# Kernel optimization log

Hardware: AMD Instinct MI355X
Metric: run time of the kernel (lower is better)

Reference implementation:

```python
import jax, jax.numpy as jnp
import numpy as np


def setup_inputs() -> dict:
    key = jax.random.key(0)
    k1, k2 = jax.random.split(key)
    # [1, D, H, W, C] cubic feature volume
    image_features = jax.random.normal(k1, (1, 64, 64, 64, 64), dtype=jnp.float32)
    # [1, N, 3] vertex coords in the original 128^3 volume, in [0, 128)
    graph_features = jax.random.uniform(k2, (1, 200000, 3), dtype=jnp.float32) * 128.0
    return {"image_features": image_features, "graph_features": graph_features}


def reference(image_features, graph_features):
    img = image_features[0]                      # [D, H, W, C]
    H = img.shape[0]
    factor = jnp.float32(128.0 / H)
    x = graph_features[..., -3] / factor         # [B, N]
    y = graph_features[..., -2] / factor
    z = graph_features[..., -1] / factor
    hm1 = jnp.float32(H - 1)
    x1 = jnp.floor(x); x2 = jnp.minimum(jnp.ceil(x), hm1)
    y1 = jnp.floor(y); y2 = jnp.minimum(jnp.ceil(y), hm1)
    z1 = jnp.floor(z); z2 = jnp.minimum(jnp.ceil(z), hm1)

    def gather(ix, iy, iz):
        # [B, N] index arrays -> [B, N, C] gathered features
        return img[ix.astype(jnp.int32), iy.astype(jnp.int32), iz.astype(jnp.int32)]

    wx = (x - x1)[..., None]; wx2 = (x2 - x)[..., None]
    wy = (y - y1)[..., None]; wy2 = (y2 - y)[..., None]
    wz = (z - z1)[..., None]; wz2 = (z2 - z)[..., None]

    # z = z1 plane
    q11 = gather(x1, y1, z1); q21 = gather(x2, y1, z1)
    q12 = gather(x1, y2, z1); q22 = gather(x2, y2, z1)
    lerp_y1 = (q22 * wx + q12 * wx2) * wy + (q21 * wx + q11 * wx2) * wy2

    # z = z2 plane
    q11 = gather(x1, y1, z2); q21 = gather(x2, y1, z2)
    q12 = gather(x1, y2, z2); q22 = gather(x2, y2, z2)
    lerp_y2 = (q22 * wx + q12 * wx2) * wy + (q21 * wx + q11 * wx2) * wy2

    return lerp_y2 * wz + lerp_y1 * wz2          # [B, N, C]
```

## Files before the change

kernel.cpp:

```cpp
#include <hip/hip_runtime.h>


#define NBUCK   4096
#define CAP     128
#define OVCAP   8192
#define TILE_F4 2048

typedef float __attribute__((ext_vector_type(4))) fx4;

#define GLOBAL_AS __attribute__((address_space(1)))
#define LDS_AS    __attribute__((address_space(3)))

__device__ __forceinline__ void async_copy16(const float4* g, float4* l) {
    __builtin_amdgcn_global_load_lds(
        (const GLOBAL_AS unsigned int*)(const void*)g,
        (LDS_AS unsigned int*)(void*)l, 16, 0, 0);
}

__device__ __forceinline__ float4 f4mul(float4 a, float s) {
    return make_float4(a.x * s, a.y * s, a.z * s, a.w * s);
}
__device__ __forceinline__ float4 f4fma(float4 a, float s, float4 acc) {
    return make_float4(fmaf(a.x, s, acc.x), fmaf(a.y, s, acc.y),
                       fmaf(a.z, s, acc.z), fmaf(a.w, s, acc.w));
}

__global__ __launch_bounds__(256) void scatter_kernel(
    const float* __restrict__ coords, int* __restrict__ counts,
    float4* __restrict__ buckets, float4* __restrict__ overflow, int n)
{
    int p = blockIdx.x * 256 + threadIdx.x;
    if (p >= n) return;
    float xs = coords[3 * p + 0] * 0.5f;
    float ys = coords[3 * p + 1] * 0.5f;
    float zs = coords[3 * p + 2] * 0.5f;
    int vx = (int)floorf(xs), vy = (int)floorf(ys), vz = (int)floorf(zs);
    int bucket = ((vx >> 2) << 8) | ((vy >> 2) << 4) | (vz >> 2);
    int slot = atomicAdd(&counts[bucket], 1);
    float4 v = make_float4(xs, ys, zs, __int_as_float(p));
    if (slot < CAP) {
        buckets[bucket * CAP + slot] = v;
    } else {
        int o = atomicAdd(&counts[NBUCK], 1);
        if (o < OVCAP) overflow[o] = v;
    }
}

__global__ __launch_bounds__(256) void gather_kernel(
    const float* __restrict__ img, const int* __restrict__ counts,
    const float4* __restrict__ buckets, const float4* __restrict__ overflow,
    float* __restrict__ out)
{
    const float4* __restrict__ imgv = (const float4*)img;
    int cvec = threadIdx.x & 15;
    int grp  = threadIdx.x >> 4;

    if (blockIdx.x < NBUCK) {
        __shared__ float4 tile[TILE_F4];
        int bucket = (blockIdx.x & 7) * 512 + (blockIdx.x >> 3);
        int bx0 = (bucket >> 8) << 2;
        int by0 = ((bucket >> 4) & 15) << 2;
        int bz0 = (bucket & 15) << 2;

        {
            int wv   = threadIdx.x >> 6;
            int lane = threadIdx.x & 63;
            #pragma unroll
            for (int c = 0; c < 8; c++) {
                int f = ((wv << 3) + c) * 64 + lane;
                int tv = f >> 4;
                int ch = f & 15;
                tv = min(tv, 124);
                int lx = tv / 25;
                int rem = tv - lx * 25;
                int ly = rem / 5;
                int lz = rem - ly * 5;
                int gx = min(bx0 + lx, 63);
                int gy = min(by0 + ly, 63);
                int gz = min(bz0 + lz, 63);
                const float4* src = &imgv[(((((gx << 6) + gy) << 6) + gz) << 4) + ch];
                async_copy16(src, &tile[((wv << 3) + c) * 64]);
            }
        }
        int cnt = min(counts[bucket], CAP);
        __syncthreads();

        for (int i = grp; i < cnt; i += 16) {
            float4 cs = buckets[bucket * CAP + i];
            float x = cs.x, y = cs.y, z = cs.z;
            int p = __float_as_int(cs.w);

            float fx1 = floorf(x), fx2 = fminf(ceilf(x), 63.0f);
            float fy1 = floorf(y), fy2 = fminf(ceilf(y), 63.0f);
            float fz1 = floorf(z), fz2 = fminf(ceilf(z), 63.0f);

            int lx1 = (int)fx1 - bx0, lx2 = (int)fx2 - bx0;
            int ly1 = (int)fy1 - by0, ly2 = (int)fy2 - by0;
            int lz1 = (int)fz1 - bz0, lz2 = (int)fz2 - bz0;
            int ax1 = lx1 * 25, ax2 = lx2 * 25;
            int ay1 = ly1 * 5,  ay2 = ly2 * 5;

            float4 q111 = tile[((ax1 + ay1 + lz1) << 4) + cvec];
            float4 q211 = tile[((ax2 + ay1 + lz1) << 4) + cvec];
            float4 q121 = tile[((ax1 + ay2 + lz1) << 4) + cvec];
            float4 q221 = tile[((ax2 + ay2 + lz1) << 4) + cvec];
            float4 q112 = tile[((ax1 + ay1 + lz2) << 4) + cvec];
            float4 q212 = tile[((ax2 + ay1 + lz2) << 4) + cvec];
            float4 q122 = tile[((ax1 + ay2 + lz2) << 4) + cvec];
            float4 q222 = tile[((ax2 + ay2 + lz2) << 4) + cvec];

            float wx = x - fx1, wxc = fx2 - x;
            float wy = y - fy1, wyc = fy2 - y;
            float wz = z - fz1, wzc = fz2 - z;

            float4 ly1v = f4fma(f4fma(q221, wx, f4mul(q121, wxc)), wy,
                                f4mul(f4fma(q211, wx, f4mul(q111, wxc)), wyc));
            float4 ly2v = f4fma(f4fma(q222, wx, f4mul(q122, wxc)), wy,
                                f4mul(f4fma(q212, wx, f4mul(q112, wxc)), wyc));
            float4 res = f4fma(ly2v, wz, f4mul(ly1v, wzc));

            fx4 r; r.x = res.x; r.y = res.y; r.z = res.z; r.w = res.w;
            __builtin_nontemporal_store(r, (fx4*)out + (p << 4) + cvec);
        }
    } else {
        int ob = blockIdx.x - NBUCK;
        int cnt = min(counts[NBUCK], OVCAP);
        for (int i = (ob << 4) + grp; i < cnt; i += 32 * 16) {
            float4 cs = overflow[i];
            float x = cs.x, y = cs.y, z = cs.z;
            int p = __float_as_int(cs.w);

            float fx1 = floorf(x), fx2 = fminf(ceilf(x), 63.0f);
            float fy1 = floorf(y), fy2 = fminf(ceilf(y), 63.0f);
            float fz1 = floorf(z), fz2 = fminf(ceilf(z), 63.0f);

            int bx1 = ((int)fx1) << 12, bx2 = ((int)fx2) << 12;
            int by1 = ((int)fy1) << 6,  by2 = ((int)fy2) << 6;
            int iz1 = (int)fz1, iz2 = (int)fz2;

            float4 q111 = imgv[((bx1 + by1 + iz1) << 4) + cvec];
            float4 q211 = imgv[((bx2 + by1 + iz1) << 4) + cvec];
            float4 q121 = imgv[((bx1 + by2 + iz1) << 4) + cvec];
            float4 q221 = imgv[((bx2 + by2 + iz1) << 4) + cvec];
            float4 q112 = imgv[((bx1 + by1 + iz2) << 4) + cvec];
            float4 q212 = imgv[((bx2 + by1 + iz2) << 4) + cvec];
            float4 q122 = imgv[((bx1 + by2 + iz2) << 4) + cvec];
            float4 q222 = imgv[((bx2 + by2 + iz2) << 4) + cvec];

            float wx = x - fx1, wxc = fx2 - x;
            float wy = y - fy1, wyc = fy2 - y;
            float wz = z - fz1, wzc = fz2 - z;

            float4 ly1v = f4fma(f4fma(q221, wx, f4mul(q121, wxc)), wy,
                                f4mul(f4fma(q211, wx, f4mul(q111, wxc)), wyc));
            float4 ly2v = f4fma(f4fma(q222, wx, f4mul(q122, wxc)), wy,
                                f4mul(f4fma(q212, wx, f4mul(q112, wxc)), wyc));
            float4 res = f4fma(ly2v, wz, f4mul(ly1v, wzc));

            fx4 r; r.x = res.x; r.y = res.y; r.z = res.z; r.w = res.w;
            __builtin_nontemporal_store(r, (fx4*)out + (p << 4) + cvec);
        }
    }
}

__global__ __launch_bounds__(256) void trilerp_kernel(
    const float* __restrict__ img, const float* __restrict__ coords,
    float* __restrict__ out, int n_points)
{
    int tid = blockIdx.x * 256 + threadIdx.x;
    int p = tid >> 4;
    if (p >= n_points) return;
    int cvec = tid & 15;

    float x = coords[3 * p + 0] * 0.5f;
    float y = coords[3 * p + 1] * 0.5f;
    float z = coords[3 * p + 2] * 0.5f;

    float fx1 = floorf(x), fx2 = fminf(ceilf(x), 63.0f);
    float fy1 = floorf(y), fy2 = fminf(ceilf(y), 63.0f);
    float fz1 = floorf(z), fz2 = fminf(ceilf(z), 63.0f);

    float wx = x - fx1, wxc = fx2 - x;
    float wy = y - fy1, wyc = fy2 - y;
    float wz = z - fz1, wzc = fz2 - z;

    const float4* __restrict__ imgv = (const float4*)img;
    int bx1 = ((int)fx1) << 12, bx2 = ((int)fx2) << 12;
    int by1 = ((int)fy1) << 6,  by2 = ((int)fy2) << 6;
    int iz1 = (int)fz1, iz2 = (int)fz2;

    float4 q11 = imgv[((bx1 + by1 + iz1) << 4) + cvec];
    float4 q21 = imgv[((bx2 + by1 + iz1) << 4) + cvec];
    float4 q12 = imgv[((bx1 + by2 + iz1) << 4) + cvec];
    float4 q22 = imgv[((bx2 + by2 + iz1) << 4) + cvec];
    float4 ly1 = f4fma(f4fma(q22, wx, f4mul(q12, wxc)), wy,
                       f4mul(f4fma(q21, wx, f4mul(q11, wxc)), wyc));

    q11 = imgv[((bx1 + by1 + iz2) << 4) + cvec];
    q21 = imgv[((bx2 + by1 + iz2) << 4) + cvec];
    q12 = imgv[((bx1 + by2 + iz2) << 4) + cvec];
    q22 = imgv[((bx2 + by2 + iz2) << 4) + cvec];
    float4 ly2 = f4fma(f4fma(q22, wx, f4mul(q12, wxc)), wy,
                       f4mul(f4fma(q21, wx, f4mul(q11, wxc)), wyc));

    float4 res = f4fma(ly2, wz, f4mul(ly1, wzc));
    ((float4*)out)[(p << 4) + cvec] = res;
}

extern "C" void kernel_launch(void* const* d_in, const int* in_sizes, int n_in,
                              void* d_out, int out_size, void* d_ws, size_t ws_size,
                              hipStream_t stream) {
    const float* img    = (const float*)d_in[0];
    const float* coords = (const float*)d_in[1];
    float* out = (float*)d_out;
    int n = in_sizes[1] / 3;

    size_t counts_bytes = 32768;
    size_t buckets_off  = counts_bytes;
    size_t buckets_bytes = (size_t)NBUCK * CAP * sizeof(float4);
    size_t overflow_off = buckets_off + buckets_bytes;
    size_t need = overflow_off + (size_t)OVCAP * sizeof(float4);

    if (ws_size >= need) {
        int*    counts   = (int*)d_ws;
        float4* buckets  = (float4*)((char*)d_ws + buckets_off);
        float4* overflow = (float4*)((char*)d_ws + overflow_off);

        hipMemsetAsync(counts, 0, (NBUCK + 1) * sizeof(int), stream);
        int pgrid = (n + 255) / 256;
        scatter_kernel<<<pgrid, 256, 0, stream>>>(coords, counts, buckets, overflow, n);
        gather_kernel<<<NBUCK + 32, 256, 0, stream>>>(img, counts, buckets, overflow, out);
    } else {
        int threads = n * 16;
        int grid = (threads + 255) / 256;
        trilerp_kernel<<<grid, 256, 0, stream>>>(img, coords, out, n);
    }
}
```

Measured before the change: 142.0 us.

## Make gather blocks persistent over eight buckets with double-buffered async LDS staging

Each gather block now handles eight consecutive buckets with 512 threads, staging the next bucket's 5x5x5 voxel tile into a second LDS buffer while the current bucket is interpolated. Manual vmcnt waits and barriers replace the per-block __syncthreads. The aim is to hide the global-to-LDS load latency and cut per-block launch and setup overhead. In exchange the grid is much smaller (544 blocks instead of 4128), the LDS footprint doubles, and correctness relies on the hand-written waitcnt count. The trilinear code on the overflow and fallback paths is moved into a shared helper.

```diff
diff --git a/kernel.cpp b/kernel.cpp
--- a/kernel.cpp
+++ b/kernel.cpp
@@ -5,6 +5,8 @@
 #define CAP     128
 #define OVCAP   8192
 #define TILE_F4 2048
+#define NGB     512
+#define NB_PER  8
 
 typedef float __attribute__((ext_vector_type(4))) fx4;
 
@@ -46,7 +48,70 @@
     }
 }
 
-__global__ __launch_bounds__(256) void gather_kernel(
+__device__ __forceinline__ void stage_bucket(
+    const float4* __restrict__ imgv, int bucket, float4* dst,
+    int wv, int lane)
+{
+    int bx0 = (bucket >> 8) << 2;
+    int by0 = ((bucket >> 4) & 15) << 2;
+    int bz0 = (bucket & 15) << 2;
+    #pragma unroll
+    for (int c = 0; c < 4; c++) {
+        int chunk = (wv << 2) + c;
+        int f = chunk * 64 + lane;
+        int tv = min(f >> 4, 124);
+        int ch = f & 15;
+        int lx = tv / 25;
+        int rem = tv - lx * 25;
+        int ly = rem / 5;
+        int lz = rem - ly * 5;
+        int gx = min(bx0 + lx, 63);
+        int gy = min(by0 + ly, 63);
+        int gz = min(bz0 + lz, 63);
+        const float4* src = &imgv[(((((gx << 6) + gy) << 6) + gz) << 4) + ch];
+        async_copy16(src, dst + chunk * 64);
+    }
+}
+
+__device__ __forceinline__ void lerp_global_store(
+    const float4* __restrict__ imgv, float4 cs, int cvec,
+    float* __restrict__ out)
+{
+    float x = cs.x, y = cs.y, z = cs.z;
+    int p = __float_as_int(cs.w);
+
+    float fx1 = floorf(x), fx2 = fminf(ceilf(x), 63.0f);
+    float fy1 = floorf(y), fy2 = fminf(ceilf(y), 63.0f);
+    float fz1 = floorf(z), fz2 = fminf(ceilf(z), 63.0f);
+
+    int bx1 = ((int)fx1) << 12, bx2 = ((int)fx2) << 12;
+    int by1 = ((int)fy1) << 6,  by2 = ((int)fy2) << 6;
+    int iz1 = (int)fz1, iz2 = (int)fz2;
+
+    float4 q111 = imgv[((bx1 + by1 + iz1) << 4) + cvec];
+    float4 q211 = imgv[((bx2 + by1 + iz1) << 4) + cvec];
+    float4 q121 = imgv[((bx1 + by2 + iz1) << 4) + cvec];
+    float4 q221 = imgv[((bx2 + by2 + iz1) << 4) + cvec];
+    float4 q112 = imgv[((bx1 + by1 + iz2) << 4) + cvec];
+    float4 q212 = imgv[((bx2 + by1 + iz2) << 4) + cvec];
+    float4 q122 = imgv[((bx1 + by2 + iz2) << 4) + cvec];
+    float4 q222 = imgv[((bx2 + by2 + iz2) << 4) + cvec];
+
+    float wx = x - fx1, wxc = fx2 - x;
+    float wy = y - fy1, wyc = fy2 - y;
+    float wz = z - fz1, wzc = fz2 - z;
+
+    float4 ly1v = f4fma(f4fma(q221, wx, f4mul(q121, wxc)), wy,
+                        f4mul(f4fma(q211, wx, f4mul(q111, wxc)), wyc));
+    float4 ly2v = f4fma(f4fma(q222, wx, f4mul(q122, wxc)), wy,
+                        f4mul(f4fma(q212, wx, f4mul(q112, wxc)), wyc));
+    float4 res = f4fma(ly2v, wz, f4mul(ly1v, wzc));
+
+    fx4 r; r.x = res.x; r.y = res.y; r.z = res.z; r.w = res.w;
+    __builtin_nontemporal_store(r, (fx4*)out + (p << 4) + cvec);
+}
+
+__global__ __launch_bounds__(512) void gather_kernel(
     const float* __restrict__ img, const int* __restrict__ counts,
     const float4* __restrict__ buckets, const float4* __restrict__ overflow,
     float* __restrict__ out)
@@ -55,110 +120,77 @@
     int cvec = threadIdx.x & 15;
     int grp  = threadIdx.x >> 4;
 
-    if (blockIdx.x < NBUCK) {
-        __shared__ float4 tile[TILE_F4];
-        int bucket = (blockIdx.x & 7) * 512 + (blockIdx.x >> 3);
-        int bx0 = (bucket >> 8) << 2;
-        int by0 = ((bucket >> 4) & 15) << 2;
-        int bz0 = (bucket & 15) << 2;
-
-        {
-            int wv   = threadIdx.x >> 6;
-            int lane = threadIdx.x & 63;
-            #pragma unroll
-            for (int c = 0; c < 8; c++) {
-                int f = ((wv << 3) + c) * 64 + lane;
-                int tv = f >> 4;
-                int ch = f & 15;
-                tv = min(tv, 124);
-                int lx = tv / 25;
-                int rem = tv - lx * 25;
-                int ly = rem / 5;
-                int lz = rem - ly * 5;
-                int gx = min(bx0 + lx, 63);
-                int gy = min(by0 + ly, 63);
-                int gz = min(bz0 + lz, 63);
-                const float4* src = &imgv[(((((gx << 6) + gy) << 6) + gz) << 4) + ch];
-                async_copy16(src, &tile[((wv << 3) + c) * 64]);
+    if (blockIdx.x < NGB) {
+        __shared__ float4 tile[2][TILE_F4];
+        int wv   = threadIdx.x >> 6;
+        int lane = threadIdx.x & 63;
+        int bbase = (blockIdx.x & 7) * 512 + (blockIdx.x >> 3) * NB_PER;
+
+        stage_bucket(imgv, bbase, tile[0], wv, lane);
+
+        for (int i = 0; i < NB_PER; ++i) {
+            float4* cur = tile[i & 1];
+            if (i + 1 < NB_PER) {
+                stage_bucket(imgv, bbase + i + 1, tile[(i + 1) & 1], wv, lane);
+                asm volatile("s_waitcnt vmcnt(4)" ::: "memory");
+            } else {
+                asm volatile("s_waitcnt vmcnt(0)" ::: "memory");
             }
-        }
-        int cnt = min(counts[bucket], CAP);
-        __syncthreads();
-
-        for (int i = grp; i < cnt; i += 16) {
-            float4 cs = buckets[bucket * CAP + i];
-            float x = cs.x, y = cs.y, z = cs.z;
-            int p = __float_as_int(cs.w);
-
-            float fx1 = floorf(x), fx2 = fminf(ceilf(x), 63.0f);
-            float fy1 = floorf(y), fy2 = fminf(ceilf(y), 63.0f);
-            float fz1 = floorf(z), fz2 = fminf(ceilf(z), 63.0f);
-
-            int lx1 = (int)fx1 - bx0, lx2 = (int)fx2 - bx0;
-            int ly1 = (int)fy1 - by0, ly2 = (int)fy2 - by0;
-            int lz1 = (int)fz1 - bz0, lz2 = (int)fz2 - bz0;
-            int ax1 = lx1 * 25, ax2 = lx2 * 25;
-            int ay1 = ly1 * 5,  ay2 = ly2 * 5;
-
-            float4 q111 = tile[((ax1 + ay1 + lz1) << 4) + cvec];
-            float4 q211 = tile[((ax2 + ay1 + lz1) << 4) + cvec];
-            float4 q121 = tile[((ax1 + ay2 + lz1) << 4) + cvec];
-            float4 q221 = tile[((ax2 + ay2 + lz1) << 4) + cvec];
-            float4 q112 = tile[((ax1 + ay1 + lz2) << 4) + cvec];
-            float4 q212 = tile[((ax2 + ay1 + lz2) << 4) + cvec];
-            float4 q122 = tile[((ax1 + ay2 + lz2) << 4) + cvec];
-            float4 q222 = tile[((ax2 + ay2 + lz2) << 4) + cvec];
-
-            float wx = x - fx1, wxc = fx2 - x;
-            float wy = y - fy1, wyc = fy2 - y;
-            float wz = z - fz1, wzc = fz2 - z;
-
-            float4 ly1v = f4fma(f4fma(q221, wx, f4mul(q121, wxc)), wy,
-                                f4mul(f4fma(q211, wx, f4mul(q111, wxc)), wyc));
-            float4 ly2v = f4fma(f4fma(q222, wx, f4mul(q122, wxc)), wy,
-                                f4mul(f4fma(q212, wx, f4mul(q112, wxc)), wyc));
-            float4 res = f4fma(ly2v, wz, f4mul(ly1v, wzc));
-
-            fx4 r; r.x = res.x; r.y = res.y; r.z = res.z; r.w = res.w;
-            __builtin_nontemporal_store(r, (fx4*)out + (p << 4) + cvec);
+            __builtin_amdgcn_s_barrier();
+            asm volatile("" ::: "memory");
+
+            int bucket = bbase + i;
+            int bx0 = (bucket >> 8) << 2;
+            int by0 = ((bucket >> 4) & 15) << 2;
+            int bz0 = (bucket & 15) << 2;
+            int cnt = min(counts[bucket], CAP);
+
+            for (int t = grp; t < cnt; t += 32) {
+                float4 cs = buckets[bucket * CAP + t];
+                float x = cs.x, y = cs.y, z = cs.z;
+                int p = __float_as_int(cs.w);
+
+                float fx1 = floorf(x), fx2 = fminf(ceilf(x), 63.0f);
+                float fy1 = floorf(y), fy2 = fminf(ceilf(y), 63.0f);
+                float fz1 = floorf(z), fz2 = fminf(ceilf(z), 63.0f);
+
+                int lx1 = (int)fx1 - bx0, lx2 = (int)fx2 - bx0;
+                int ly1 = (int)fy1 - by0, ly2 = (int)fy2 - by0;
+                int lz1 = (int)fz1 - bz0, lz2 = (int)fz2 - bz0;
+                int ax1 = lx1 * 25, ax2 = lx2 * 25;
+                int ay1 = ly1 * 5,  ay2 = ly2 * 5;
+
+                float4 q111 = cur[((ax1 + ay1 + lz1) << 4) + cvec];
+                float4 q211 = cur[((ax2 + ay1 + lz1) << 4) + cvec];
+                float4 q121 = cur[((ax1 + ay2 + lz1) << 4) + cvec];
+                float4 q221 = cur[((ax2 + ay2 + lz1) << 4) + cvec];
+                float4 q112 = cur[((ax1 + ay1 + lz2) << 4) + cvec];
+                float4 q212 = cur[((ax2 + ay1 + lz2) << 4) + cvec];
+                float4 q122 = cur[((ax1 + ay2 + lz2) << 4) + cvec];
+                float4 q222 = cur[((ax2 + ay2 + lz2) << 4) + cvec];
+
+                float wx = x - fx1, wxc = fx2 - x;
+                float wy = y - fy1, wyc = fy2 - y;
+                float wz = z - fz1, wzc = fz2 - z;
+
+                float4 ly1v = f4fma(f4fma(q221, wx, f4mul(q121, wxc)), wy,
+                                    f4mul(f4fma(q211, wx, f4mul(q111, wxc)), wyc));
+                float4 ly2v = f4fma(f4fma(q222, wx, f4mul(q122, wxc)), wy,
+                                    f4mul(f4fma(q212, wx, f4mul(q112, wxc)), wyc));
+                float4 res = f4fma(ly2v, wz, f4mul(ly1v, wzc));
+
+                fx4 r; r.x = res.x; r.y = res.y; r.z = res.z; r.w = res.w;
+                __builtin_nontemporal_store(r, (fx4*)out + (p << 4) + cvec);
+            }
+            asm volatile("" ::: "memory");
+            __builtin_amdgcn_s_barrier();
         }
     } else {
-        int ob = blockIdx.x - NBUCK;
+        int ob = blockIdx.x - NGB;
         int cnt = min(counts[NBUCK], OVCAP);
-        for (int i = (ob << 4) + grp; i < cnt; i += 32 * 16) {
+        for (int i = (ob << 5) + grp; i < cnt; i += 32 * 32) {
             float4 cs = overflow[i];
-            float x = cs.x, y = cs.y, z = cs.z;
-            int p = __float_as_int(cs.w);
-
-            float fx1 = floorf(x), fx2 = fminf(ceilf(x), 63.0f);
-            float fy1 = floorf(y), fy2 = fminf(ceilf(y), 63.0f);
-            float fz1 = floorf(z), fz2 = fminf(ceilf(z), 63.0f);
-
-            int bx1 = ((int)fx1) << 12, bx2 = ((int)fx2) << 12;
-            int by1 = ((int)fy1) << 6,  by2 = ((int)fy2) << 6;
-            int iz1 = (int)fz1, iz2 = (int)fz2;
-
-            float4 q111 = imgv[((bx1 + by1 + iz1) << 4) + cvec];
-            float4 q211 = imgv[((bx2 + by1 + iz1) << 4) + cvec];
-            float4 q121 = imgv[((bx1 + by2 + iz1) << 4) + cvec];
-            float4 q221 = imgv[((bx2 + by2 + iz1) << 4) + cvec];
-            float4 q112 = imgv[((bx1 + by1 + iz2) << 4) + cvec];
-            float4 q212 = imgv[((bx2 + by1 + iz2) << 4) + cvec];
-            float4 q122 = imgv[((bx1 + by2 + iz2) << 4) + cvec];
-            float4 q222 = imgv[((bx2 + by2 + iz2) << 4) + cvec];
-
-            float wx = x - fx1, wxc = fx2 - x;
-            float wy = y - fy1, wyc = fy2 - y;
-            float wz = z - fz1, wzc = fz2 - z;
-
-            float4 ly1v = f4fma(f4fma(q221, wx, f4mul(q121, wxc)), wy,
-                                f4mul(f4fma(q211, wx, f4mul(q111, wxc)), wyc));
-            float4 ly2v = f4fma(f4fma(q222, wx, f4mul(q122, wxc)), wy,
-                                f4mul(f4fma(q212, wx, f4mul(q112, wxc)), wyc));
-            float4 res = f4fma(ly2v, wz, f4mul(ly1v, wzc));
-
-            fx4 r; r.x = res.x; r.y = res.y; r.z = res.z; r.w = res.w;
-            __builtin_nontemporal_store(r, (fx4*)out + (p << 4) + cvec);
+            lerp_global_store(imgv, cs, cvec, out);
         }
     }
 }
@@ -176,35 +208,8 @@
     float y = coords[3 * p + 1] * 0.5f;
     float z = coords[3 * p + 2] * 0.5f;
 
-    float fx1 = floorf(x), fx2 = fminf(ceilf(x), 63.0f);
-    float fy1 = floorf(y), fy2 = fminf(ceilf(y), 63.0f);
-    float fz1 = floorf(z), fz2 = fminf(ceilf(z), 63.0f);
-
-    float wx = x - fx1, wxc = fx2 - x;
-    float wy = y - fy1, wyc = fy2 - y;
-    float wz = z - fz1, wzc = fz2 - z;
-
-    const float4* __restrict__ imgv = (const float4*)img;
-    int bx1 = ((int)fx1) << 12, bx2 = ((int)fx2) << 12;
-    int by1 = ((int)fy1) << 6,  by2 = ((int)fy2) << 6;
-    int iz1 = (int)fz1, iz2 = (int)fz2;
-
-    float4 q11 = imgv[((bx1 + by1 + iz1) << 4) + cvec];
-    float4 q21 = imgv[((bx2 + by1 + iz1) << 4) + cvec];
-    float4 q12 = imgv[((bx1 + by2 + iz1) << 4) + cvec];
-    float4 q22 = imgv[((bx2 + by2 + iz1) << 4) + cvec];
-    float4 ly1 = f4fma(f4fma(q22, wx, f4mul(q12, wxc)), wy,
-                       f4mul(f4fma(q21, wx, f4mul(q11, wxc)), wyc));
-
-    q11 = imgv[((bx1 + by1 + iz2) << 4) + cvec];
-    q21 = imgv[((bx2 + by1 + iz2) << 4) + cvec];
-    q12 = imgv[((bx1 + by2 + iz2) << 4) + cvec];
-    q22 = imgv[((bx2 + by2 + iz2) << 4) + cvec];
-    float4 ly2 = f4fma(f4fma(q22, wx, f4mul(q12, wxc)), wy,
-                       f4mul(f4fma(q21, wx, f4mul(q11, wxc)), wyc));
-
-    float4 res = f4fma(ly2, wz, f4mul(ly1, wzc));
-    ((float4*)out)[(p << 4) + cvec] = res;
+    float4 cs = make_float4(x, y, z, __int_as_float(p));
+    lerp_global_store((const float4*)img, cs, cvec, out);
 }
 
 extern "C" void kernel_launch(void* const* d_in, const int* in_sizes, int n_in,
@@ -229,7 +234,7 @@
         hipMemsetAsync(counts, 0, (NBUCK + 1) * sizeof(int), stream);
         int pgrid = (n + 255) / 256;
         scatter_kernel<<<pgrid, 256, 0, stream>>>(coords, counts, buckets, overflow, n);
-        gather_kernel<<<NBUCK + 32, 256, 0, stream>>>(img, counts, buckets, overflow, out);
+        gather_kernel<<<NGB + 32, 512, 0, stream>>>(img, counts, buckets, overflow, out);
     } else {
         int threads = n * 16;
         int grid = (threads + 255) / 256;
```

New measurement: 144.6 us. Within noise of the previous version (+1.8%).
